# Optimization experiments

Hardware: AMD Instinct MI355X
Metric: run time of the kernel (lower is better)

## Reference

```python
import jax, jax.numpy as jnp
import numpy as np
from jax import lax

WS = 8   # window size
NH = 8   # num heads
EPS = 1e-5  # BatchNorm eps (eval mode, running mean=0 var=1)

def _rel_pos_index(ws):
    coords = np.stack(np.meshgrid(np.arange(ws), np.arange(ws), indexing='ij'))
    cf = coords.reshape(2, -1)
    rel = (cf[:, :, None] - cf[:, None, :]).transpose(1, 2, 0).astype(np.int64)
    rel[..., 0] += ws - 1
    rel[..., 1] += ws - 1
    rel[..., 0] *= 2 * ws - 1
    return rel.sum(-1)  # [ws*ws, ws*ws]

REL_IDX = _rel_pos_index(WS)

def conv2d(x, w, b=None, pad=0, groups=1):
    y = lax.conv_general_dilated(x, w, (1, 1), [(pad, pad), (pad, pad)],
                                 dimension_numbers=('NCHW', 'OIHW', 'NCHW'),
                                 feature_group_count=groups)
    if b is not None:
        y = y + b[None, :, None, None]
    return y

def bn(x, g, b):
    # eval-mode BatchNorm with running_mean=0, running_var=1
    scale = g / np.float32(np.sqrt(1.0 + EPS))
    return x * scale[None, :, None, None] + b[None, :, None, None]

def avgpool(x, kh, kw, ph, pw):
    # PyTorch AvgPool2d: zero padding, count_include_pad=True -> divide by kernel size
    s = lax.reduce_window(x, 0.0, lax.add, (1, 1, kh, kw), (1, 1, 1, 1),
                          [(0, 0), (0, 0), (ph, ph), (pw, pw)])
    return s / (kh * kw)

def setup_inputs() -> dict:
    key = jax.random.key(0)
    ks = jax.random.split(key, 8)
    C = 256
    x = jax.random.normal(ks[0], (8, C, 128, 128), dtype=jnp.float32)
    qkv_w = jax.random.normal(ks[1], (3 * C, C, 1, 1), dtype=jnp.float32) * 0.05
    qkv_b = jnp.zeros((3 * C,), jnp.float32)
    local_w = jax.random.normal(ks[2], (C, C // NH, 3, 3), dtype=jnp.float32) * 0.05
    local_b = jnp.zeros((C,), jnp.float32)
    rpb_table = jax.random.normal(ks[3], ((2 * WS - 1) ** 2, NH), dtype=jnp.float32) * 0.02
    proj_dw_w = jax.random.normal(ks[4], (C, 1, 3, 3), dtype=jnp.float32) * 0.05
    proj_dw_b = jnp.zeros((C,), jnp.float32)
    proj_pw_w = jax.random.normal(ks[5], (C, C, 1, 1), dtype=jnp.float32) * 0.05
    proj_pw_b = jnp.zeros((C,), jnp.float32)
    return {
        'x': x, 'qkv_w': qkv_w, 'qkv_b': qkv_b,
        'local_w': local_w, 'local_b': local_b,
        'local_bn_g': jnp.ones((C,), jnp.float32), 'local_bn_b': jnp.zeros((C,), jnp.float32),
        'rpb_table': rpb_table,
        'proj_dw_w': proj_dw_w, 'proj_dw_b': proj_dw_b,
        'proj_bn_g': jnp.ones((C,), jnp.float32), 'proj_bn_b': jnp.zeros((C,), jnp.float32),
        'proj_pw_w': proj_pw_w, 'proj_pw_b': proj_pw_b,
    }

def reference(x, qkv_w, qkv_b, local_w, local_b, local_bn_g, local_bn_b,
              rpb_table, proj_dw_w, proj_dw_b, proj_bn_g, proj_bn_b,
              proj_pw_w, proj_pw_b):
    B, C, H, W = x.shape
    hd = C // NH
    scale = hd ** -0.5
    # local branch: grouped 3x3 conv (groups=num_heads) + BN + ReLU
    local = jax.nn.relu(bn(conv2d(x, local_w, local_b, pad=1, groups=NH),
                           local_bn_g, local_bn_b))
    # H, W divisible by WS -> self.pad (reflect) is a no-op
    qkv = conv2d(x, qkv_w, qkv_b)  # [B, 3C, H, W]
    Hh, Ww = H // WS, W // WS
    # 'b (qkv h d) (hh ws1) (ww ws2) -> qkv (b hh ww) h (ws1 ws2) d'
    qkv = qkv.reshape(B, 3, NH, hd, Hh, WS, Ww, WS)
    qkv = qkv.transpose(1, 0, 4, 6, 2, 5, 7, 3).reshape(3, B * Hh * Ww, NH, WS * WS, hd)
    q, k, v = qkv[0], qkv[1], qkv[2]
    dots = jnp.einsum('bhid,bhjd->bhij', q, k) * scale  # [Bwin, NH, 64, 64]
    bias = rpb_table[REL_IDX.reshape(-1)].reshape(WS * WS, WS * WS, NH).transpose(2, 0, 1)
    attn = jax.nn.softmax(dots + bias[None], axis=-1)
    out = jnp.einsum('bhij,bhjd->bhid', attn, v)
    # '(b hh ww) h (ws1 ws2) d -> b (h d) (hh ws1) (ww ws2)'
    out = out.reshape(B, Hh, Ww, NH, WS, WS, hd).transpose(0, 3, 6, 1, 4, 2, 5).reshape(B, C, H, W)
    # asymmetric avg-pool fusion with reflect pre-pad
    ax = avgpool(jnp.pad(out, ((0, 0), (0, 0), (0, 1), (0, 0)), mode='reflect'),
                 WS, 1, WS // 2 - 1, 0)
    ay = avgpool(jnp.pad(out, ((0, 0), (0, 0), (0, 0), (0, 1)), mode='reflect'),
                 1, WS, 0, WS // 2 - 1)
    out = ax + ay + local
    # pad_out: reflect (0,1,0,1)
    out = jnp.pad(out, ((0, 0), (0, 0), (0, 1), (0, 1)), mode='reflect')
    # SeparableConvBN proj: depthwise 3x3 -> BN -> pointwise 1x1
    out = conv2d(out, proj_dw_w, proj_dw_b, pad=1, groups=C)
    out = bn(out, proj_bn_g, proj_bn_b)
    out = conv2d(out, proj_pw_w, proj_pw_b)
    return out[:, :, :H, :W]
```

## Files before the change

kernel.cpp:

```cpp
#include <hip/hip_runtime.h>
#include <cstddef>

#define C_ 256
#define H_ 128
#define W_ 128
#define HW_ 16384
#define NH_ 8
#define NWIN_ 256
#define EPS_ 1e-5f

typedef short s16x8 __attribute__((ext_vector_type(8)));
typedef float f32x4 __attribute__((ext_vector_type(4)));

__device__ inline void bf16_split(float f, short& h, short& l) {
  unsigned u = __float_as_uint(f);
  unsigned hb = (u + 0x7FFFu + ((u >> 16) & 1u)) >> 16;
  float hf = __uint_as_float(hb << 16);
  h = (short)hb;
  float r = f - hf;
  unsigned v = __float_as_uint(r);
  unsigned lb = (v + 0x7FFFu + ((v >> 16) & 1u)) >> 16;
  l = (short)lb;
}

__global__ __launch_bounds__(256) void k1_qkv_mfma(
    const float* __restrict__ xb, const float* __restrict__ wq,
    const float* __restrict__ bias, float* __restrict__ qkv_s) {
  __shared__ short s_a[2][128][40];
  __shared__ short s_b[2][128][40];
  const int tid = threadIdx.x;
  const int y   = blockIdx.x;
  const int oc0 = blockIdx.y * 128;

  const int lane = tid & 63;
  const int wid  = tid >> 6;
  const int m0w = (wid >> 1) * 64;
  const int n0w = (wid & 1) * 64;

  f32x4 acc[4][4];
#pragma unroll
  for (int i = 0; i < 4; ++i)
#pragma unroll
    for (int j = 0; j < 4; ++j) acc[i][j] = f32x4{0.f, 0.f, 0.f, 0.f};

  const int pcol = tid & 127;
  const int kq0  = tid >> 7;

  for (int k0 = 0; k0 < 256; k0 += 32) {
#pragma unroll
    for (int i = 0; i < 4; ++i) {
      const int ff = tid + i * 256;
      const int row = ff >> 3;
      const int c4 = ff & 7;
      const float4 w4 = *reinterpret_cast<const float4*>(
          &wq[(size_t)(oc0 + row) * 256 + k0 + c4 * 4]);
      short h0, h1, h2, h3, l0, l1, l2, l3;
      bf16_split(w4.x, h0, l0);
      bf16_split(w4.y, h1, l1);
      bf16_split(w4.z, h2, l2);
      bf16_split(w4.w, h3, l3);
      *reinterpret_cast<short4*>(&s_a[0][row][c4 * 4]) = make_short4(h0, h1, h2, h3);
      *reinterpret_cast<short4*>(&s_a[1][row][c4 * 4]) = make_short4(l0, l1, l2, l3);
    }
#pragma unroll
    for (int it = 0; it < 4; ++it) {
      const int kq = kq0 * 4 + it;
      short h[4], l[4];
#pragma unroll
      for (int e = 0; e < 4; ++e) {
        const float v = xb[(size_t)(k0 + kq * 4 + e) * HW_ + y * W_ + pcol];
        bf16_split(v, h[e], l[e]);
      }
      *reinterpret_cast<short4*>(&s_b[0][pcol][kq * 4]) = make_short4(h[0], h[1], h[2], h[3]);
      *reinterpret_cast<short4*>(&s_b[1][pcol][kq * 4]) = make_short4(l[0], l[1], l[2], l[3]);
    }
    __syncthreads();

    const int mr = lane & 15;
    const int kg = (lane >> 4) * 8;
    s16x8 ah[4], al[4], bh[4], bl[4];
#pragma unroll
    for (int fm = 0; fm < 4; ++fm) {
      ah[fm] = *reinterpret_cast<const s16x8*>(&s_a[0][m0w + fm * 16 + mr][kg]);
      al[fm] = *reinterpret_cast<const s16x8*>(&s_a[1][m0w + fm * 16 + mr][kg]);
    }
#pragma unroll
    for (int fn = 0; fn < 4; ++fn) {
      bh[fn] = *reinterpret_cast<const s16x8*>(&s_b[0][n0w + fn * 16 + mr][kg]);
      bl[fn] = *reinterpret_cast<const s16x8*>(&s_b[1][n0w + fn * 16 + mr][kg]);
    }
#pragma unroll
    for (int fm = 0; fm < 4; ++fm)
#pragma unroll
      for (int fn = 0; fn < 4; ++fn) {
        acc[fm][fn] = __builtin_amdgcn_mfma_f32_16x16x32_bf16(
            ah[fm], bh[fn], acc[fm][fn], 0, 0, 0);
        acc[fm][fn] = __builtin_amdgcn_mfma_f32_16x16x32_bf16(
            ah[fm], bl[fn], acc[fm][fn], 0, 0, 0);
        acc[fm][fn] = __builtin_amdgcn_mfma_f32_16x16x32_bf16(
            al[fm], bh[fn], acc[fm][fn], 0, 0, 0);
      }
    __syncthreads();
  }

  const int mr4 = (lane >> 4) * 4;
  const int nn  = lane & 15;
  const int hh = y >> 3, ws1 = y & 7;
#pragma unroll
  for (int fm = 0; fm < 4; ++fm) {
    const int oc = oc0 + m0w + fm * 16 + mr4;
    const float4 b4 = *reinterpret_cast<const float4*>(&bias[oc]);
    const int qkvi = oc >> 8;
    const int head = (oc >> 5) & 7;
    const int d0 = oc & 31;
#pragma unroll
    for (int fn = 0; fn < 4; ++fn) {
      const int x = n0w + fn * 16 + nn;
      const int win = hh * 16 + (x >> 3);
      const int pos = ws1 * 8 + (x & 7);
      const size_t addr =
          ((((size_t)qkvi * NWIN_ + win) * NH_ + head) * 64 + pos) * 32 + d0;
      float4 v;
      v.x = acc[fm][fn].x + b4.x;
      v.y = acc[fm][fn].y + b4.y;
      v.z = acc[fm][fn].z + b4.z;
      v.w = acc[fm][fn].w + b4.w;
      *reinterpret_cast<float4*>(&qkv_s[addr]) = v;
    }
  }
}

__global__ __launch_bounds__(256) void k2_wt(
    const float* __restrict__ lw, short* __restrict__ WT) {
  const int i = blockIdx.x * 256 + threadIdx.x;
  if (i >= 73728) return;
  const int g = i / 9216;
  const int rem = i % 9216;
  const int tau = rem / 1024;
  const int oc = (rem >> 5) & 31;
  const int ic = rem & 31;
  const float w = lw[((size_t)(g * 32 + oc) * 32 + ic) * 9 + tau];
  short h, l;
  bf16_split(w, h, l);
  WT[((g * 9 + tau) * 2 + 0) * 1024 + oc * 32 + ic] = h;
  WT[((g * 9 + tau) * 2 + 1) * 1024 + oc * 32 + ic] = l;
}

__global__ __launch_bounds__(256) void k2_mfma(
    const float* __restrict__ x, const short* __restrict__ WT,
    const float* __restrict__ lb, const float* __restrict__ bng,
    const float* __restrict__ bnb, float* __restrict__ local_buf) {
  __shared__ short xt[3][132][64];
  const int tid = threadIdx.x;
  const int y = blockIdx.x;
  const int g = blockIdx.y;
  const int bb = blockIdx.z;

  for (int i = tid; i < 12480; i += 256) {
    const int r = i / 4160;
    const int rem = i - r * 4160;
    const int ic = rem / 130;
    const int px = rem - ic * 130 - 1;
    const int gy = y + r - 1;
    float v = 0.f;
    if (gy >= 0 && gy < H_ && px >= 0 && px < W_)
      v = x[(((size_t)(bb * C_ + g * 32 + ic)) * H_ + gy) * W_ + px];
    short h, l;
    bf16_split(v, h, l);
    const int slot = px + 1;
    const int sw = (slot & 7) * 8;
    xt[r][slot][(ic) ^ sw] = h;
    xt[r][slot][(32 + ic) ^ sw] = l;
  }
  __syncthreads();

  const int lane = tid & 63;
  const int wid = tid >> 6;
  const int px0w = wid * 32;
  const int mr = lane & 15;
  const int kg = (lane >> 4) * 8;

  f32x4 acc[2][2];
#pragma unroll
  for (int i = 0; i < 2; ++i)
#pragma unroll
    for (int j = 0; j < 2; ++j) acc[i][j] = f32x4{0.f, 0.f, 0.f, 0.f};

#pragma unroll
  for (int tau = 0; tau < 9; ++tau) {
    const int dy = tau / 3;
    const int dx = tau % 3;
    const int wt0 = ((g * 9 + tau) * 2) * 1024;
    s16x8 ah[2], al[2], bh[2], bl[2];
#pragma unroll
    for (int fm = 0; fm < 2; ++fm) {
      ah[fm] = *reinterpret_cast<const s16x8*>(&WT[wt0 + (fm * 16 + mr) * 32 + kg]);
      al[fm] = *reinterpret_cast<const s16x8*>(&WT[wt0 + 1024 + (fm * 16 + mr) * 32 + kg]);
    }
#pragma unroll
    for (int fn = 0; fn < 2; ++fn) {
      const int slot = px0w + fn * 16 + mr + dx;
      const int sw = (slot & 7) * 8;
      bh[fn] = *reinterpret_cast<const s16x8*>(&xt[dy][slot][(kg) ^ sw]);
      bl[fn] = *reinterpret_cast<const s16x8*>(&xt[dy][slot][(32 + kg) ^ sw]);
    }
#pragma unroll
    for (int fm = 0; fm < 2; ++fm)
#pragma unroll
      for (int fn = 0; fn < 2; ++fn) {
        acc[fm][fn] = __builtin_amdgcn_mfma_f32_16x16x32_bf16(
            ah[fm], bh[fn], acc[fm][fn], 0, 0, 0);
        acc[fm][fn] = __builtin_amdgcn_mfma_f32_16x16x32_bf16(
            ah[fm], bl[fn], acc[fm][fn], 0, 0, 0);
        acc[fm][fn] = __builtin_amdgcn_mfma_f32_16x16x32_bf16(
            al[fm], bh[fn], acc[fm][fn], 0, 0, 0);
      }
  }

  const int mr4 = (lane >> 4) * 4;
  const float inv_s = 1.0f / sqrtf(1.0f + EPS_);
#pragma unroll
  for (int fm = 0; fm < 2; ++fm)
#pragma unroll
    for (int r = 0; r < 4; ++r) {
      const int c = g * 32 + fm * 16 + mr4 + r;
      const float scale = bng[c] * inv_s;
      const float cb = lb[c], sb = bnb[c];
#pragma unroll
      for (int fn = 0; fn < 2; ++fn) {
        const int px = px0w + fn * 16 + mr;
        const float val = fmaxf(fmaf(acc[fm][fn][r] + cb, scale, sb), 0.f);
        local_buf[(((size_t)(bb * C_ + c)) * H_ + y) * W_ + px] = val;
      }
    }
}

__global__ __launch_bounds__(128) void k3_attn(
    const float* __restrict__ qkv_s, const float* __restrict__ rpb,
    float* __restrict__ attn_s) {
  __shared__ float kvs[2][2][64 * 32];
  __shared__ float rpb_s[225 * 8];
  const int tid = threadIdx.x;
  const int wid = tid >> 6, lane = tid & 63;
  const int pid = blockIdx.x * 2 + wid;
  const int win = pid >> 3, h = pid & 7;
  const int hh = win >> 4, ww = win & 15;

  for (int i = tid; i < 225 * 8; i += 128) rpb_s[i] = rpb[i];

  const size_t qbase = (((size_t)0 * NWIN_ + win) * NH_ + h) * 2048;
  const size_t kbase = (((size_t)1 * NWIN_ + win) * NH_ + h) * 2048;
  const size_t vbase = (((size_t)2 * NWIN_ + win) * NH_ + h) * 2048;

  float* Kl = kvs[wid][0];
  float* Vl = kvs[wid][1];
#pragma unroll
  for (int r = 0; r < 8; ++r) {
    const int e = r * 256 + lane * 4;
    *reinterpret_cast<float4*>(&Kl[e]) =
        *reinterpret_cast<const float4*>(&qkv_s[kbase + e]);
    *reinterpret_cast<float4*>(&Vl[e]) =
        *reinterpret_cast<const float4*>(&qkv_s[vbase + e]);
  }
  float4 qreg[8];
#pragma unroll
  for (int dd = 0; dd < 8; ++dd)
    qreg[dd] = *reinterpret_cast<const float4*>(&qkv_s[qbase + lane * 32 + dd * 4]);

  __syncthreads();

  float s[64];
#pragma unroll
  for (int j = 0; j < 64; ++j) {
    const float* kr = &Kl[j * 32];
    float sj = 0.f;
#pragma unroll
    for (int dd = 0; dd < 8; ++dd) {
      const float4 kv = *reinterpret_cast<const float4*>(&kr[dd * 4]);
      sj = fmaf(qreg[dd].x, kv.x, sj);
      sj = fmaf(qreg[dd].y, kv.y, sj);
      sj = fmaf(qreg[dd].z, kv.z, sj);
      sj = fmaf(qreg[dd].w, kv.w, sj);
    }
    s[j] = sj;
  }

  const float scale = 0.17677669529663687f;
  const int r1 = lane >> 3, c1 = lane & 7;
  float m = -1e30f;
#pragma unroll
  for (int j = 0; j < 64; ++j) {
    const int jr = j >> 3, jc = j & 7;
    const int idx = (r1 - jr + 7) * 15 + (c1 - jc + 7);
    s[j] = fmaf(s[j], scale, rpb_s[idx * 8 + h]);
    m = fmaxf(m, s[j]);
  }
  float sum = 0.f;
#pragma unroll
  for (int j = 0; j < 64; ++j) {
    s[j] = __expf(s[j] - m);
    sum += s[j];
  }
  const float inv = 1.0f / sum;

  float o[32];
#pragma unroll
  for (int d = 0; d < 32; ++d) o[d] = 0.f;
#pragma unroll
  for (int j = 0; j < 64; ++j) {
    const float pj = s[j] * inv;
    const float* vr = &Vl[j * 32];
#pragma unroll
    for (int dd = 0; dd < 8; ++dd) {
      const float4 vv = *reinterpret_cast<const float4*>(&vr[dd * 4]);
      o[dd * 4 + 0] = fmaf(pj, vv.x, o[dd * 4 + 0]);
      o[dd * 4 + 1] = fmaf(pj, vv.y, o[dd * 4 + 1]);
      o[dd * 4 + 2] = fmaf(pj, vv.z, o[dd * 4 + 2]);
      o[dd * 4 + 3] = fmaf(pj, vv.w, o[dd * 4 + 3]);
    }
  }

  const int yy = hh * 8 + r1, xx = ww * 8 + c1;
  const size_t obase = ((size_t)(h * 32) * H_ + yy) * W_ + xx;
#pragma unroll
  for (int d = 0; d < 32; ++d) attn_s[obase + (size_t)d * HW_] = o[d];
}

__global__ __launch_bounds__(256) void k4_pool(
    const float* __restrict__ attn_s, float* __restrict__ localpool) {
  const int bid = blockIdx.x;
  const int c = bid >> 6;
  const int rp = bid & 63;
  const int i = rp * 2 + (threadIdx.x >> 7);
  const int j = threadIdx.x & 127;
  const float* ap = attn_s + (size_t)c * HW_;
  float sx = 0.f;
#pragma unroll
  for (int dr = -3; dr <= 4; ++dr) {
    int r = i + dr;
    if (r < 0 || r > 128) continue;
    if (r == 128) r = 126;
    sx += ap[r * W_ + j];
  }
  float sy = 0.f;
#pragma unroll
  for (int dc = -3; dc <= 4; ++dc) {
    int cc = j + dc;
    if (cc < 0 || cc > 128) continue;
    if (cc == 128) cc = 126;
    sy += ap[i * W_ + cc];
  }
  const size_t idx = (size_t)c * HW_ + i * W_ + j;
  localpool[idx] = (sx + sy) * 0.125f + localpool[idx];
}

__global__ __launch_bounds__(256) void k5_dw(
    const float* __restrict__ pool, const float* __restrict__ dww,
    const float* __restrict__ dwb, const float* __restrict__ bng,
    const float* __restrict__ bnb, float* __restrict__ dwout) {
  const int bid = blockIdx.x;
  const int c = bid >> 6;
  const int rp = bid & 63;
  const int i = rp * 2 + (threadIdx.x >> 7);
  const int j = threadIdx.x & 127;
  const float* pp = pool + (size_t)c * HW_;
  const float* wp = dww + c * 9;
  float acc = 0.f;
#pragma unroll
  for (int dy = 0; dy < 3; ++dy) {
    int r = i + dy - 1;
    if (r < 0) continue;
    if (r == 128) r = 126;
#pragma unroll
    for (int dx = 0; dx < 3; ++dx) {
      int cc = j + dx - 1;
      if (cc < 0) continue;
      if (cc == 128) cc = 126;
      acc = fmaf(wp[dy * 3 + dx], pp[r * W_ + cc], acc);
    }
  }
  const float scale = bng[c] / sqrtf(1.0f + EPS_);
  dwout[(size_t)c * HW_ + i * W_ + j] = fmaf(acc + dwb[c], scale, bnb[c]);
}

__global__ __launch_bounds__(256) void k6_pw_mfma(
    const float* __restrict__ xin, const float* __restrict__ wq,
    const float* __restrict__ bias, float* __restrict__ outb) {
  __shared__ short s_a[2][128][40];
  __shared__ short s_b[2][128][40];
  const int tid = threadIdx.x;
  const int y   = blockIdx.x;
  const int oc0 = blockIdx.y * 128;

  const int lane = tid & 63;
  const int wid  = tid >> 6;
  const int m0w = (wid >> 1) * 64;
  const int n0w = (wid & 1) * 64;

  f32x4 acc[4][4];
#pragma unroll
  for (int i = 0; i < 4; ++i)
#pragma unroll
    for (int j = 0; j < 4; ++j) acc[i][j] = f32x4{0.f, 0.f, 0.f, 0.f};

  const int pcol = tid & 127;
  const int kq0  = tid >> 7;

  for (int k0 = 0; k0 < 256; k0 += 32) {
#pragma unroll
    for (int i = 0; i < 4; ++i) {
      const int ff = tid + i * 256;
      const int row = ff >> 3;
      const int c4 = ff & 7;
      const float4 w4 = *reinterpret_cast<const float4*>(
          &wq[(size_t)(oc0 + row) * 256 + k0 + c4 * 4]);
      short h0, h1, h2, h3, l0, l1, l2, l3;
      bf16_split(w4.x, h0, l0);
      bf16_split(w4.y, h1, l1);
      bf16_split(w4.z, h2, l2);
      bf16_split(w4.w, h3, l3);
      *reinterpret_cast<short4*>(&s_a[0][row][c4 * 4]) = make_short4(h0, h1, h2, h3);
      *reinterpret_cast<short4*>(&s_a[1][row][c4 * 4]) = make_short4(l0, l1, l2, l3);
    }
#pragma unroll
    for (int it = 0; it < 4; ++it) {
      const int kq = kq0 * 4 + it;
      short h[4], l[4];
#pragma unroll
      for (int e = 0; e < 4; ++e) {
        const float v = xin[(size_t)(k0 + kq * 4 + e) * HW_ + y * W_ + pcol];
        bf16_split(v, h[e], l[e]);
      }
      *reinterpret_cast<short4*>(&s_b[0][pcol][kq * 4]) = make_short4(h[0], h[1], h[2], h[3]);
      *reinterpret_cast<short4*>(&s_b[1][pcol][kq * 4]) = make_short4(l[0], l[1], l[2], l[3]);
    }
    __syncthreads();

    const int mr = lane & 15;
    const int kg = (lane >> 4) * 8;
    s16x8 ah[4], al[4], bh[4], bl[4];
#pragma unroll
    for (int fm = 0; fm < 4; ++fm) {
      ah[fm] = *reinterpret_cast<const s16x8*>(&s_a[0][m0w + fm * 16 + mr][kg]);
      al[fm] = *reinterpret_cast<const s16x8*>(&s_a[1][m0w + fm * 16 + mr][kg]);
    }
#pragma unroll
    for (int fn = 0; fn < 4; ++fn) {
      bh[fn] = *reinterpret_cast<const s16x8*>(&s_b[0][n0w + fn * 16 + mr][kg]);
      bl[fn] = *reinterpret_cast<const s16x8*>(&s_b[1][n0w + fn * 16 + mr][kg]);
    }
#pragma unroll
    for (int fm = 0; fm < 4; ++fm)
#pragma unroll
      for (int fn = 0; fn < 4; ++fn) {
        acc[fm][fn] = __builtin_amdgcn_mfma_f32_16x16x32_bf16(
            ah[fm], bh[fn], acc[fm][fn], 0, 0, 0);
        acc[fm][fn] = __builtin_amdgcn_mfma_f32_16x16x32_bf16(
            ah[fm], bl[fn], acc[fm][fn], 0, 0, 0);
        acc[fm][fn] = __builtin_amdgcn_mfma_f32_16x16x32_bf16(
            al[fm], bh[fn], acc[fm][fn], 0, 0, 0);
      }
    __syncthreads();
  }

  const int mr4 = (lane >> 4) * 4;
  const int nn  = lane & 15;
#pragma unroll
  for (int fm = 0; fm < 4; ++fm) {
    const int ocb = oc0 + m0w + fm * 16 + mr4;
#pragma unroll
    for (int r = 0; r < 4; ++r) {
      const int oc = ocb + r;
      const float bo = bias[oc];
#pragma unroll
      for (int fn = 0; fn < 4; ++fn) {
        const int px = n0w + fn * 16 + nn;
        outb[(size_t)oc * HW_ + y * W_ + px] = acc[fm][fn][r] + bo;
      }
    }
  }
}

extern "C" void kernel_launch(void* const* d_in, const int* in_sizes, int n_in,
                              void* d_out, int out_size, void* d_ws, size_t ws_size,
                              hipStream_t stream) {
  const float* x          = (const float*)d_in[0];
  const float* qkv_w      = (const float*)d_in[1];
  const float* qkv_b      = (const float*)d_in[2];
  const float* local_w    = (const float*)d_in[3];
  const float* local_b    = (const float*)d_in[4];
  const float* local_bn_g = (const float*)d_in[5];
  const float* local_bn_b = (const float*)d_in[6];
  const float* rpb        = (const float*)d_in[7];
  const float* proj_dw_w  = (const float*)d_in[8];
  const float* proj_dw_b  = (const float*)d_in[9];
  const float* proj_bn_g  = (const float*)d_in[10];
  const float* proj_bn_b  = (const float*)d_in[11];
  const float* proj_pw_w  = (const float*)d_in[12];
  const float* proj_pw_b  = (const float*)d_in[13];
  float* out = (float*)d_out;
  float* ws = (float*)d_ws;

  const size_t CHW = (size_t)C_ * HW_;
  const size_t NEED = 12 * CHW * 4;
  if (ws_size < NEED) return;

  float* local_all = ws;
  float* qkv_s     = ws + 8 * CHW;
  float* attn_s    = qkv_s + 3 * CHW;
  short* WT = (short*)qkv_s;

  k2_wt<<<dim3(288), 256, 0, stream>>>(local_w, WT);
  k2_mfma<<<dim3(128, 8, 8), 256, 0, stream>>>(
      x, WT, local_b, local_bn_g, local_bn_b, local_all);

  for (int bb = 0; bb < 8; ++bb) {
    const float* xb = x + (size_t)bb * CHW;
    float* outb = out + (size_t)bb * CHW;
    float* local_s = local_all + (size_t)bb * CHW;
    k1_qkv_mfma<<<dim3(128, 6), 256, 0, stream>>>(xb, qkv_w, qkv_b, qkv_s);
    k3_attn<<<dim3(1024), 128, 0, stream>>>(qkv_s, rpb, attn_s);
    k4_pool<<<dim3(C_ * 64), 256, 0, stream>>>(attn_s, local_s);
    k5_dw<<<dim3(C_ * 64), 256, 0, stream>>>(local_s, proj_dw_w, proj_dw_b,
                                             proj_bn_g, proj_bn_b, attn_s);
    k6_pw_mfma<<<dim3(128, 2), 256, 0, stream>>>(attn_s, proj_pw_w, proj_pw_b, outb);
  }
}
```

Before: 1.914 ms.

## Vectorize k2 input staging, remap k2 blocks per XCD, halve k6 OC tile

The k2 local-conv kernel now loads input rows with float4 reads and zeroes only the two halo slots, instead of scalar loads with per-element bounds checks. Its grid is flattened to 1D and remapped so that each XCD handles contiguous (batch, group) pairs, which should improve L2 locality of x. Separately, the k6 pointwise GEMM tile shrinks from 128 to 64 output channels, doubling its grid to 512 blocks so more CUs are busy per batch. The trade-off is that each k6 block reloads the input row tile for half as many output channels, so input traffic goes up.

```diff
diff --git a/kernel.cpp b/kernel.cpp
--- a/kernel.cpp
+++ b/kernel.cpp
@@ -152,25 +152,45 @@
     const float* __restrict__ bnb, float* __restrict__ local_buf) {
   __shared__ short xt[3][132][64];
   const int tid = threadIdx.x;
-  const int y = blockIdx.x;
-  const int g = blockIdx.y;
-  const int bb = blockIdx.z;
-
-  for (int i = tid; i < 12480; i += 256) {
-    const int r = i / 4160;
-    const int rem = i - r * 4160;
-    const int ic = rem / 130;
-    const int px = rem - ic * 130 - 1;
+  const int wg = blockIdx.x;
+  const int xcd = wg & 7;
+  const int jj = wg >> 3;
+  const int pair = xcd * 8 + (jj >> 7);
+  const int y = jj & 127;
+  const int g = pair & 7;
+  const int bb = pair >> 3;
+
+  if (tid < 192) {
+    const int r = tid >> 6;
+    const int k = tid & 63;
+    const int side = k >> 5, ic = k & 31;
+    const int slot = side ? 129 : 0;
+    const int sw = (slot & 7) * 8;
+    xt[r][slot][ic ^ sw] = 0;
+    xt[r][slot][(32 + ic) ^ sw] = 0;
+  }
+  const int pxq = tid & 31;
+#pragma unroll
+  for (int it = 0; it < 12; ++it) {
+    const int q = it * 8 + (tid >> 5);
+    const int r = q >> 5;
+    const int ic = q & 31;
     const int gy = y + r - 1;
-    float v = 0.f;
-    if (gy >= 0 && gy < H_ && px >= 0 && px < W_)
-      v = x[(((size_t)(bb * C_ + g * 32 + ic)) * H_ + gy) * W_ + px];
-    short h, l;
-    bf16_split(v, h, l);
-    const int slot = px + 1;
-    const int sw = (slot & 7) * 8;
-    xt[r][slot][(ic) ^ sw] = h;
-    xt[r][slot][(32 + ic) ^ sw] = l;
+    const int px = pxq * 4;
+    float4 v = make_float4(0.f, 0.f, 0.f, 0.f);
+    if (gy >= 0 && gy < H_)
+      v = *reinterpret_cast<const float4*>(
+          &x[(((size_t)(bb * C_ + g * 32 + ic)) * H_ + gy) * W_ + px]);
+#pragma unroll
+    for (int e = 0; e < 4; ++e) {
+      const float f = (&v.x)[e];
+      short h, l;
+      bf16_split(f, h, l);
+      const int slot = px + 1 + e;
+      const int sw = (slot & 7) * 8;
+      xt[r][slot][ic ^ sw] = h;
+      xt[r][slot][(32 + ic) ^ sw] = l;
+    }
   }
   __syncthreads();
 
@@ -386,20 +406,20 @@
 __global__ __launch_bounds__(256) void k6_pw_mfma(
     const float* __restrict__ xin, const float* __restrict__ wq,
     const float* __restrict__ bias, float* __restrict__ outb) {
-  __shared__ short s_a[2][128][40];
+  __shared__ short s_a[2][64][40];
   __shared__ short s_b[2][128][40];
   const int tid = threadIdx.x;
   const int y   = blockIdx.x;
-  const int oc0 = blockIdx.y * 128;
+  const int oc0 = blockIdx.y * 64;
 
   const int lane = tid & 63;
   const int wid  = tid >> 6;
-  const int m0w = (wid >> 1) * 64;
+  const int m0w = (wid >> 1) * 32;
   const int n0w = (wid & 1) * 64;
 
-  f32x4 acc[4][4];
-#pragma unroll
-  for (int i = 0; i < 4; ++i)
+  f32x4 acc[2][4];
+#pragma unroll
+  for (int i = 0; i < 2; ++i)
 #pragma unroll
     for (int j = 0; j < 4; ++j) acc[i][j] = f32x4{0.f, 0.f, 0.f, 0.f};
 
@@ -408,7 +428,7 @@
 
   for (int k0 = 0; k0 < 256; k0 += 32) {
 #pragma unroll
-    for (int i = 0; i < 4; ++i) {
+    for (int i = 0; i < 2; ++i) {
       const int ff = tid + i * 256;
       const int row = ff >> 3;
       const int c4 = ff & 7;
@@ -438,9 +458,9 @@
 
     const int mr = lane & 15;
     const int kg = (lane >> 4) * 8;
-    s16x8 ah[4], al[4], bh[4], bl[4];
-#pragma unroll
-    for (int fm = 0; fm < 4; ++fm) {
+    s16x8 ah[2], al[2], bh[4], bl[4];
+#pragma unroll
+    for (int fm = 0; fm < 2; ++fm) {
       ah[fm] = *reinterpret_cast<const s16x8*>(&s_a[0][m0w + fm * 16 + mr][kg]);
       al[fm] = *reinterpret_cast<const s16x8*>(&s_a[1][m0w + fm * 16 + mr][kg]);
     }
@@ -450,7 +470,7 @@
       bl[fn] = *reinterpret_cast<const s16x8*>(&s_b[1][n0w + fn * 16 + mr][kg]);
     }
 #pragma unroll
-    for (int fm = 0; fm < 4; ++fm)
+    for (int fm = 0; fm < 2; ++fm)
 #pragma unroll
       for (int fn = 0; fn < 4; ++fn) {
         acc[fm][fn] = __builtin_amdgcn_mfma_f32_16x16x32_bf16(
@@ -466,7 +486,7 @@
   const int mr4 = (lane >> 4) * 4;
   const int nn  = lane & 15;
 #pragma unroll
-  for (int fm = 0; fm < 4; ++fm) {
+  for (int fm = 0; fm < 2; ++fm) {
     const int ocb = oc0 + m0w + fm * 16 + mr4;
 #pragma unroll
     for (int r = 0; r < 4; ++r) {
@@ -511,7 +531,7 @@
   short* WT = (short*)qkv_s;
 
   k2_wt<<<dim3(288), 256, 0, stream>>>(local_w, WT);
-  k2_mfma<<<dim3(128, 8, 8), 256, 0, stream>>>(
+  k2_mfma<<<dim3(8192), 256, 0, stream>>>(
       x, WT, local_b, local_bn_g, local_bn_b, local_all);
 
   for (int bb = 0; bb < 8; ++bb) {
@@ -523,6 +543,6 @@
     k4_pool<<<dim3(C_ * 64), 256, 0, stream>>>(attn_s, local_s);
     k5_dw<<<dim3(C_ * 64), 256, 0, stream>>>(local_s, proj_dw_w, proj_dw_b,
                                              proj_bn_g, proj_bn_b, attn_s);
-    k6_pw_mfma<<<dim3(128, 2), 256, 0, stream>>>(attn_s, proj_pw_w, proj_pw_b, outb);
-  }
-}
+    k6_pw_mfma<<<dim3(128, 4), 256, 0, stream>>>(attn_s, proj_pw_w, proj_pw_b, outb);
+  }
+}
```

Result: faster. 1.742 ms (-9.0%).
